# Performance work log

Hardware: AMD Instinct MI355X
Metric: run time of the kernel (lower is better)

The kernel has to match this reference:

```python
import jax, jax.numpy as jnp
import numpy as np

N_NODES = 50000
N_EDGES = 600000
D = 128
REL_DIM = 100
N_REL = 40
NEG_SLOPE = 0.2


def setup_inputs() -> dict:
    key = jax.random.key(0)
    ks = jax.random.split(key, 9)
    return {
        "node_features": jax.random.normal(ks[0], (N_NODES, D), jnp.float32),
        "edge_index": jax.random.randint(ks[1], (2, N_EDGES), 0, N_NODES, jnp.int64 if jax.config.jax_enable_x64 else jnp.int32),
        "edge_type": jax.random.randint(ks[2], (N_EDGES,), 0, N_REL, jnp.int32),
        "W": jax.random.normal(ks[3], (D, D), jnp.float32) * (1.0 / np.sqrt(D)),
        "W_r": jax.random.normal(ks[4], (REL_DIM, D), jnp.float32) * (1.0 / np.sqrt(REL_DIM)),
        "a": jax.random.normal(ks[5], (3 * D,), jnp.float32) * (1.0 / np.sqrt(3 * D)),
        "W_res": jax.random.normal(ks[6], (D, D), jnp.float32) * (1.0 / np.sqrt(D)),
        "b_res": jax.random.normal(ks[7], (D,), jnp.float32) * 0.01,
        "rel_emb": jax.random.normal(ks[8], (N_REL, REL_DIM), jnp.float32),
    }


def _segment_softmax(logits, seg_ids, num_segments):
    # numerically stable softmax over edges grouped by destination node
    seg_max = jax.ops.segment_max(logits, seg_ids, num_segments=num_segments)
    seg_max = jnp.where(jnp.isfinite(seg_max), seg_max, 0.0)
    e = jnp.exp(logits - seg_max[seg_ids])
    seg_sum = jax.ops.segment_sum(e, seg_ids, num_segments=num_segments)
    return e / (seg_sum[seg_ids] + 1e-16)


def reference(node_features, edge_index, edge_type, W, W_r, a, W_res, b_res, rel_emb):
    src = edge_index[0]  # x_j (source / message sender)
    dst = edge_index[1]  # x_i (target / aggregation index)

    h = node_features @ W                      # [N, D]
    h_rel = rel_emb[edge_type] @ W_r           # [E, D]
    h_src = h[src]                             # [E, D]
    h_dst = h[dst]                             # [E, D]

    # attention logit per edge: a . cat(W x_i, W x_j, W_r r_e), LeakyReLU(0.2)
    logit = h_dst @ a[:D] + h_src @ a[D:2 * D] + h_rel @ a[2 * D:]  # [E]
    logit = jax.nn.leaky_relu(logit, NEG_SLOPE)

    alpha = _segment_softmax(logit, dst, N_NODES)  # [E]

    agg = jax.ops.segment_sum(h_src * alpha[:, None], dst, num_segments=N_NODES)  # [N, D]

    out = agg + node_features @ W_res + b_res  # residual connection
    # LayerG: SELU then dropout (identity in eval mode)
    return jax.nn.selu(out)
```

## Files before the change

kernel.cpp:

```cpp
#include <hip/hip_runtime.h>
#include <hip/hip_bf16.h>

typedef __attribute__((ext_vector_type(8))) short bf16x8;
typedef __attribute__((ext_vector_type(4))) float f32x4;

#define LDS_STRIDE 528
#define CAP 64

__device__ __forceinline__ float waveSum(float v) {
    for (int d = 32; d; d >>= 1) v += __shfl_xor(v, d, 64);
    return v;
}
__device__ __forceinline__ unsigned short f2bf(float f) {
    union { float f; unsigned int u; } v; v.f = f;
    unsigned int r = (v.u + 0x7FFF + ((v.u >> 16) & 1)) >> 16;
    return (unsigned short)r;
}
__device__ __forceinline__ float bf2f(unsigned int hbits) {
    union { unsigned int u; float f; } v; v.u = hbits << 16;
    return v.f;
}

__global__ __launch_bounds__(256) void setup_kernel(
    int* __restrict__ counts, int N,
    const float* __restrict__ W, const float* __restrict__ W_res,
    unsigned short* __restrict__ WbPack,
    const float* __restrict__ W_r, const float* __restrict__ a,
    const float* __restrict__ rel_emb, float* __restrict__ rl,
    int n_rel, int rel_dim, int zb)
{
    __shared__ float a3[128];
    __shared__ float wa[128];
    int bid = blockIdx.x;
    int tid = threadIdx.x;
    if (bid < zb) {
        int i = bid * 256 + tid;
        if (i < N) counts[i] = 0;
        return;
    }
    if (bid < zb + 16) {
        int g = (bid - zb) * 256 + tid;
        int t = g >> 8;
        int s = (g >> 6) & 3;
        int lane = g & 63;
        int ncol = ((t & 7) << 4) + (lane & 15);
        int k0 = s * 32 + ((lane >> 4) << 3);
        const float* srcw = (t < 8) ? W : W_res;
        unsigned short* dst = WbPack + ((size_t)(t * 4 + s) * 64 + lane) * 8;
        #pragma unroll
        for (int j = 0; j < 8; ++j) dst[j] = f2bf(srcw[(size_t)(k0 + j) * 128 + ncol]);
        return;
    }
    if (tid < 128) {
        a3[tid] = a[256 + tid];
    }
    __syncthreads();
    if (tid < rel_dim) {
        float s = 0.f;
        for (int d = 0; d < 128; ++d) s += W_r[tid * 128 + d] * a3[d];
        wa[tid] = s;
    }
    __syncthreads();
    if (tid < n_rel) {
        float s = 0.f;
        for (int k = 0; k < rel_dim; ++k) s += rel_emb[tid * rel_dim + k] * wa[k];
        rl[tid] = s;
    }
}

__global__ __launch_bounds__(256) void gemm_dual_kernel(
    const float* __restrict__ X, const unsigned short* __restrict__ WbPack,
    const float* __restrict__ b_res, const float* __restrict__ a,
    unsigned short* __restrict__ hb, unsigned short* __restrict__ resb,
    float* __restrict__ p, float* __restrict__ q, int M)
{
    __shared__ __align__(16) unsigned char smem[64 * LDS_STRIDE];
    __shared__ float pq_s[128];
    const int tid = threadIdx.x;
    const int lane = tid & 63;
    const int wave = tid >> 6;
    const int rowbase = blockIdx.x * 64;
    const int c16 = lane & 15;
    const int kq = lane >> 4;

    if (tid < 128) pq_s[tid] = 0.f;

    bf16x8 wfrag[4][4];
    #pragma unroll
    for (int tt = 0; tt < 4; ++tt)
        #pragma unroll
        for (int s = 0; s < 4; ++s)
            wfrag[tt][s] = *(const bf16x8*)(WbPack + ((size_t)((wave * 4 + tt) * 4 + s) * 64 + lane) * 8);

    float bres[4];
    #pragma unroll
    for (int tt = 0; tt < 4; ++tt) {
        int t = wave * 4 + tt;
        bres[tt] = (t >= 8) ? b_res[(t - 8) * 16 + c16] : 0.f;
    }
    float pa[4], qa[4];
    #pragma unroll
    for (int tt = 0; tt < 4; ++tt) {
        int col = (wave * 4 + tt) * 16 + c16;
        pa[tt] = (wave < 2) ? a[col] : 0.f;
        qa[tt] = (wave < 2) ? a[128 + col] : 0.f;
    }

    #pragma unroll
    for (int j = 0; j < 8; ++j) {
        int ch = j * 256 + tid;
        int r = ch >> 5;
        int c = ch & 31;
        int gr = rowbase + r; if (gr >= M) gr = M - 1;
        float4 v = *(const float4*)(X + (size_t)gr * 128 + c * 4);
        unsigned int u0 = ((unsigned)f2bf(v.y) << 16) | f2bf(v.x);
        unsigned int u1 = ((unsigned)f2bf(v.w) << 16) | f2bf(v.z);
        *(uint2*)(smem + r * LDS_STRIDE + c * 8) = make_uint2(u0, u1);
    }
    __syncthreads();

    f32x4 acc[4][4];
    #pragma unroll
    for (int rt = 0; rt < 4; ++rt)
        #pragma unroll
        for (int tt = 0; tt < 4; ++tt) acc[rt][tt] = (f32x4){0.f, 0.f, 0.f, 0.f};

    #pragma unroll
    for (int s = 0; s < 4; ++s) {
        #pragma unroll
        for (int rt = 0; rt < 4; ++rt) {
            int row = rt * 16 + c16;
            bf16x8 af = *(const bf16x8*)(smem + row * LDS_STRIDE + s * 64 + kq * 16);
            #pragma unroll
            for (int tt = 0; tt < 4; ++tt)
                acc[rt][tt] = __builtin_amdgcn_mfma_f32_16x16x32_bf16(af, wfrag[tt][s], acc[rt][tt], 0, 0, 0);
        }
    }
    __syncthreads();

    if (wave < 2) {
        #pragma unroll
        for (int rt = 0; rt < 4; ++rt) {
            #pragma unroll
            for (int i = 0; i < 4; ++i) {
                float pp = 0.f, qq = 0.f;
                #pragma unroll
                for (int tt = 0; tt < 4; ++tt) {
                    pp += acc[rt][tt][i] * pa[tt];
                    qq += acc[rt][tt][i] * qa[tt];
                }
                #pragma unroll
                for (int d = 1; d < 16; d <<= 1) {
                    pp += __shfl_xor(pp, d, 64);
                    qq += __shfl_xor(qq, d, 64);
                }
                if (c16 == 0) {
                    int r = rt * 16 + kq * 4 + i;
                    atomicAdd(&pq_s[r], pp);
                    atomicAdd(&pq_s[64 + r], qq);
                }
            }
        }
    }

    #pragma unroll
    for (int rt = 0; rt < 4; ++rt) {
        #pragma unroll
        for (int tt = 0; tt < 4; ++tt) {
            int colall = (wave * 4 + tt) * 16 + c16;
            #pragma unroll
            for (int i = 0; i < 4; ++i) {
                int row = rt * 16 + kq * 4 + i;
                *(unsigned short*)(smem + row * LDS_STRIDE + colall * 2) = f2bf(acc[rt][tt][i] + bres[tt]);
            }
        }
    }
    __syncthreads();

    #pragma unroll
    for (int j = 0; j < 4; ++j) {
        int ch = j * 256 + tid;
        int r = ch >> 4;
        int c = ch & 15;
        int gr = rowbase + r;
        uint4 hv = *(const uint4*)(smem + r * LDS_STRIDE + c * 16);
        uint4 rv = *(const uint4*)(smem + r * LDS_STRIDE + 256 + c * 16);
        if (gr < M) {
            *(uint4*)(hb + (size_t)gr * 128 + c * 8) = hv;
            *(uint4*)(resb + (size_t)gr * 128 + c * 8) = rv;
        }
    }
    if (tid < 64) {
        int gr = rowbase + tid;
        if (gr < M) { p[gr] = pq_s[tid]; q[gr] = pq_s[64 + tid]; }
    }
}

__global__ __launch_bounds__(256) void edge_kernel(
    const int* __restrict__ src, const int* __restrict__ dst, const int* __restrict__ etype,
    int* __restrict__ counts, unsigned int* __restrict__ slots, int E)
{
    const int xcd = blockIdx.x & 7;
    const int stripe = blockIdx.x >> 3;
    const int base = stripe * 2048 + threadIdx.x;
    #pragma unroll
    for (int k = 0; k < 8; ++k) {
        int e = base + k * 256;
        if (e < E) {
            int d = dst[e];
            if (((d >> 2) & 7) == xcd) {
                int s = src[e];
                int t = etype[e];
                int rk = atomicAdd(&counts[d], 1);
                if (rk < CAP)
                    slots[(size_t)d * CAP + rk] = (unsigned int)s | ((unsigned int)t << 16);
            }
        }
    }
}

__global__ __launch_bounds__(256) void agg_kernel(
    const unsigned short* __restrict__ hb, const unsigned short* __restrict__ resb,
    const float* __restrict__ p, const float* __restrict__ q, const float* __restrict__ rl,
    const int* __restrict__ counts, const unsigned int* __restrict__ slots,
    float* __restrict__ out, int N, int n_rel)
{
    __shared__ float rls[64];
    if (threadIdx.x < n_rel) rls[threadIdx.x] = rl[threadIdx.x];
    __syncthreads();

    int node = blockIdx.x * 4 + (threadIdx.x >> 6);
    int lane = threadIdx.x & 63;
    if (node >= N) return;
    int nn = min(counts[node], CAP);

    float se = 0.f;
    int sv = 0;
    if (lane < nn) {
        unsigned int pk = slots[(size_t)node * CAP + lane];
        sv = (int)(pk & 0xffffu);
        int t = (int)(pk >> 16);
        float l = p[node] + q[sv] + rls[t];
        l = (l > 0.f) ? l : 0.2f * l;
        se = __expf(l);
    }
    float ssum = waveSum(se);
    float inv = 1.0f / (ssum + 1e-16f);

    float a0 = 0.f, a1 = 0.f;
    const unsigned short* hlane = hb + lane * 2;
    int j = 0;
    for (; j + 7 < nn; j += 8) {
        float w[8]; int r[8]; unsigned int v[8];
        #pragma unroll
        for (int u = 0; u < 8; ++u) { w[u] = __shfl(se, j + u); r[u] = __shfl(sv, j + u); }
        #pragma unroll
        for (int u = 0; u < 8; ++u) v[u] = *(const unsigned int*)(hlane + (size_t)r[u] * 128);
        #pragma unroll
        for (int u = 0; u < 8; ++u) {
            a0 += w[u] * bf2f(v[u] & 0xffff);
            a1 += w[u] * bf2f(v[u] >> 16);
        }
    }
    for (; j + 3 < nn; j += 4) {
        float w[4]; int r[4]; unsigned int v[4];
        #pragma unroll
        for (int u = 0; u < 4; ++u) { w[u] = __shfl(se, j + u); r[u] = __shfl(sv, j + u); }
        #pragma unroll
        for (int u = 0; u < 4; ++u) v[u] = *(const unsigned int*)(hlane + (size_t)r[u] * 128);
        #pragma unroll
        for (int u = 0; u < 4; ++u) {
            a0 += w[u] * bf2f(v[u] & 0xffff);
            a1 += w[u] * bf2f(v[u] >> 16);
        }
    }
    for (; j < nn; ++j) {
        float w = __shfl(se, j);
        int r = __shfl(sv, j);
        unsigned int v = *(const unsigned int*)(hlane + (size_t)r * 128);
        a0 += w * bf2f(v & 0xffff);
        a1 += w * bf2f(v >> 16);
    }

    a0 *= inv; a1 *= inv;

    unsigned int rv = __builtin_nontemporal_load((const unsigned int*)(resb + (size_t)node * 128 + lane * 2));
    float o0 = a0 + bf2f(rv & 0xffff), o1 = a1 + bf2f(rv >> 16);
    const float SC = 1.0507009873554805f, AL = 1.6732632423543772f;
    o0 = (o0 > 0.f) ? SC * o0 : SC * AL * (__expf(o0) - 1.f);
    o1 = (o1 > 0.f) ? SC * o1 : SC * AL * (__expf(o1) - 1.f);
    union { float f[2]; unsigned long long u; } ov;
    ov.f[0] = o0; ov.f[1] = o1;
    __builtin_nontemporal_store(ov.u, (unsigned long long*)(out + (size_t)node * 128 + lane * 2));
}

extern "C" void kernel_launch(void* const* d_in, const int* in_sizes, int n_in,
                              void* d_out, int out_size, void* d_ws, size_t ws_size,
                              hipStream_t stream)
{
    const float* X      = (const float*)d_in[0];
    const int*   ei     = (const int*)d_in[1];
    const int*   etype  = (const int*)d_in[2];
    const float* W      = (const float*)d_in[3];
    const float* W_r    = (const float*)d_in[4];
    const float* a      = (const float*)d_in[5];
    const float* W_res  = (const float*)d_in[6];
    const float* b_res  = (const float*)d_in[7];
    const float* rel_emb= (const float*)d_in[8];

    const int N = in_sizes[0] / 128;
    const int E = in_sizes[2];
    const int n_rel = in_sizes[8] / 100;
    const int* src = ei;
    const int* dst = ei + E;

    char* w = (char*)d_ws;
    auto alloc = [&](size_t bytes) -> void* {
        void* ptr = (void*)w;
        w += (bytes + 255) & ~(size_t)255;
        return ptr;
    };
    unsigned short* WbPack = (unsigned short*)alloc((size_t)16 * 4 * 64 * 8 * 2);
    unsigned short* hb     = (unsigned short*)alloc((size_t)N * 128 * 2);
    unsigned short* resb   = (unsigned short*)alloc((size_t)N * 128 * 2);
    float* p       = (float*)alloc((size_t)N * 4);
    float* q       = (float*)alloc((size_t)N * 4);
    float* rl      = (float*)alloc(64 * 4);
    int*   counts  = (int*)alloc((size_t)N * 4);
    unsigned int* slots = (unsigned int*)alloc((size_t)N * CAP * 4);
    float* out     = (float*)d_out;

    const int zb = (N + 255) / 256;
    const int gemm_blocks = (N + 63) / 64;
    const int node_wave_blocks = (N + 3) / 4;
    const int stripes = (E + 2047) / 2048;
    const int edge_blocks = stripes * 8;

    setup_kernel<<<zb + 17, 256, 0, stream>>>(counts, N, W, W_res, WbPack,
                                              W_r, a, rel_emb, rl, n_rel, 100, zb);
    gemm_dual_kernel<<<gemm_blocks, 256, 0, stream>>>(X, WbPack, b_res, a, hb, resb, p, q, N);
    edge_kernel<<<edge_blocks, 256, 0, stream>>>(src, dst, etype, counts, slots, E);
    agg_kernel<<<node_wave_blocks, 256, 0, stream>>>(hb, resb, p, q, rl, counts, slots, out, N, n_rel);
}
```

Measured before the change: 180.9 us.

## Process two nodes per wavefront in aggregation with 32-lane half-waves

The aggregation kernel now assigns each 32-lane half of a wavefront to its own destination node. Each lane gathers 4 bf16 features (8 bytes) per neighbor instead of 2, and the softmax weights are computed in chunks of 32 edges, with the sum reduced across the half-wave. With about 12 edges per node on average, most of the 64 lanes were idle during the weight computation, and the 4-byte gathers were narrow; this change targets both. The cost is a chunk loop for nodes with more than 32 edges, and the residual load is no longer marked nontemporal.

After: 175.2 us. -3.2%, faster.

```diff
diff --git a/kernel.cpp b/kernel.cpp
--- a/kernel.cpp
+++ b/kernel.cpp
@@ -7,10 +7,6 @@
 #define LDS_STRIDE 528
 #define CAP 64
 
-__device__ __forceinline__ float waveSum(float v) {
-    for (int d = 32; d; d >>= 1) v += __shfl_xor(v, d, 64);
-    return v;
-}
 __device__ __forceinline__ unsigned short f2bf(float f) {
     union { float f; unsigned int u; } v; v.f = f;
     unsigned int r = (v.u + 0x7FFF + ((v.u >> 16) & 1)) >> 16;
@@ -229,69 +225,88 @@
     if (threadIdx.x < n_rel) rls[threadIdx.x] = rl[threadIdx.x];
     __syncthreads();
 
-    int node = blockIdx.x * 4 + (threadIdx.x >> 6);
-    int lane = threadIdx.x & 63;
+    const int tid = threadIdx.x;
+    const int lane = tid & 63;
+    const int sub = lane & 31;
+    const int shbase = lane & 32;
+    int node = blockIdx.x * 8 + ((tid >> 6) << 1) + (lane >> 5);
     if (node >= N) return;
     int nn = min(counts[node], CAP);
 
-    float se = 0.f;
-    int sv = 0;
-    if (lane < nn) {
-        unsigned int pk = slots[(size_t)node * CAP + lane];
-        sv = (int)(pk & 0xffffu);
-        int t = (int)(pk >> 16);
-        float l = p[node] + q[sv] + rls[t];
-        l = (l > 0.f) ? l : 0.2f * l;
-        se = __expf(l);
-    }
-    float ssum = waveSum(se);
+    float pnode = p[node];
+    float a0 = 0.f, a1 = 0.f, a2 = 0.f, a3 = 0.f;
+    float ssum = 0.f;
+    const unsigned short* hsub = hb + sub * 4;
+
+    for (int c = 0; c < nn; c += 32) {
+        int m = min(32, nn - c);
+        float se = 0.f;
+        int sv = 0;
+        if (sub < m) {
+            unsigned int pk = slots[(size_t)node * CAP + c + sub];
+            sv = (int)(pk & 0xffffu);
+            int t = (int)(pk >> 16);
+            float l = pnode + q[sv] + rls[t];
+            l = (l > 0.f) ? l : 0.2f * l;
+            se = __expf(l);
+        }
+        ssum += se;
+
+        int j = 0;
+        for (; j + 7 < m; j += 8) {
+            float w[8]; int r[8]; uint2 v[8];
+            #pragma unroll
+            for (int u = 0; u < 8; ++u) { w[u] = __shfl(se, shbase + j + u); r[u] = __shfl(sv, shbase + j + u); }
+            #pragma unroll
+            for (int u = 0; u < 8; ++u) v[u] = *(const uint2*)(hsub + (size_t)r[u] * 128);
+            #pragma unroll
+            for (int u = 0; u < 8; ++u) {
+                a0 += w[u] * bf2f(v[u].x & 0xffff);
+                a1 += w[u] * bf2f(v[u].x >> 16);
+                a2 += w[u] * bf2f(v[u].y & 0xffff);
+                a3 += w[u] * bf2f(v[u].y >> 16);
+            }
+        }
+        for (; j + 3 < m; j += 4) {
+            float w[4]; int r[4]; uint2 v[4];
+            #pragma unroll
+            for (int u = 0; u < 4; ++u) { w[u] = __shfl(se, shbase + j + u); r[u] = __shfl(sv, shbase + j + u); }
+            #pragma unroll
+            for (int u = 0; u < 4; ++u) v[u] = *(const uint2*)(hsub + (size_t)r[u] * 128);
+            #pragma unroll
+            for (int u = 0; u < 4; ++u) {
+                a0 += w[u] * bf2f(v[u].x & 0xffff);
+                a1 += w[u] * bf2f(v[u].x >> 16);
+                a2 += w[u] * bf2f(v[u].y & 0xffff);
+                a3 += w[u] * bf2f(v[u].y >> 16);
+            }
+        }
+        for (; j < m; ++j) {
+            float w = __shfl(se, shbase + j);
+            int r = __shfl(sv, shbase + j);
+            uint2 v = *(const uint2*)(hsub + (size_t)r * 128);
+            a0 += w * bf2f(v.x & 0xffff);
+            a1 += w * bf2f(v.x >> 16);
+            a2 += w * bf2f(v.y & 0xffff);
+            a3 += w * bf2f(v.y >> 16);
+        }
+    }
+
+    #pragma unroll
+    for (int d = 1; d < 32; d <<= 1) ssum += __shfl_xor(ssum, d, 64);
     float inv = 1.0f / (ssum + 1e-16f);
-
-    float a0 = 0.f, a1 = 0.f;
-    const unsigned short* hlane = hb + lane * 2;
-    int j = 0;
-    for (; j + 7 < nn; j += 8) {
-        float w[8]; int r[8]; unsigned int v[8];
-        #pragma unroll
-        for (int u = 0; u < 8; ++u) { w[u] = __shfl(se, j + u); r[u] = __shfl(sv, j + u); }
-        #pragma unroll
-        for (int u = 0; u < 8; ++u) v[u] = *(const unsigned int*)(hlane + (size_t)r[u] * 128);
-        #pragma unroll
-        for (int u = 0; u < 8; ++u) {
-            a0 += w[u] * bf2f(v[u] & 0xffff);
-            a1 += w[u] * bf2f(v[u] >> 16);
-        }
-    }
-    for (; j + 3 < nn; j += 4) {
-        float w[4]; int r[4]; unsigned int v[4];
-        #pragma unroll
-        for (int u = 0; u < 4; ++u) { w[u] = __shfl(se, j + u); r[u] = __shfl(sv, j + u); }
-        #pragma unroll
-        for (int u = 0; u < 4; ++u) v[u] = *(const unsigned int*)(hlane + (size_t)r[u] * 128);
-        #pragma unroll
-        for (int u = 0; u < 4; ++u) {
-            a0 += w[u] * bf2f(v[u] & 0xffff);
-            a1 += w[u] * bf2f(v[u] >> 16);
-        }
-    }
-    for (; j < nn; ++j) {
-        float w = __shfl(se, j);
-        int r = __shfl(sv, j);
-        unsigned int v = *(const unsigned int*)(hlane + (size_t)r * 128);
-        a0 += w * bf2f(v & 0xffff);
-        a1 += w * bf2f(v >> 16);
-    }
-
-    a0 *= inv; a1 *= inv;
-
-    unsigned int rv = __builtin_nontemporal_load((const unsigned int*)(resb + (size_t)node * 128 + lane * 2));
-    float o0 = a0 + bf2f(rv & 0xffff), o1 = a1 + bf2f(rv >> 16);
+    a0 *= inv; a1 *= inv; a2 *= inv; a3 *= inv;
+
+    uint2 rv = *(const uint2*)(resb + (size_t)node * 128 + sub * 4);
+    float o0 = a0 + bf2f(rv.x & 0xffff), o1 = a1 + bf2f(rv.x >> 16);
+    float o2 = a2 + bf2f(rv.y & 0xffff), o3 = a3 + bf2f(rv.y >> 16);
     const float SC = 1.0507009873554805f, AL = 1.6732632423543772f;
     o0 = (o0 > 0.f) ? SC * o0 : SC * AL * (__expf(o0) - 1.f);
     o1 = (o1 > 0.f) ? SC * o1 : SC * AL * (__expf(o1) - 1.f);
-    union { float f[2]; unsigned long long u; } ov;
-    ov.f[0] = o0; ov.f[1] = o1;
-    __builtin_nontemporal_store(ov.u, (unsigned long long*)(out + (size_t)node * 128 + lane * 2));
+    o2 = (o2 > 0.f) ? SC * o2 : SC * AL * (__expf(o2) - 1.f);
+    o3 = (o3 > 0.f) ? SC * o3 : SC * AL * (__expf(o3) - 1.f);
+    f32x4 ov = (f32x4){o0, o1, o2, o3};
+    __builtin_nontemporal_store(ov, (f32x4*)(out + (size_t)node * 128 + sub * 4));
 }
 
 extern "C" void kernel_launch(void* const* d_in, const int* in_sizes, int n_in,
@@ -332,7 +347,7 @@
 
     const int zb = (N + 255) / 256;
     const int gemm_blocks = (N + 63) / 64;
-    const int node_wave_blocks = (N + 3) / 4;
+    const int agg_blocks = (N + 7) / 8;
     const int stripes = (E + 2047) / 2048;
     const int edge_blocks = stripes * 8;
 
@@ -340,5 +355,5 @@
                                               W_r, a, rel_emb, rl, n_rel, 100, zb);
     gemm_dual_kernel<<<gemm_blocks, 256, 0, stream>>>(X, WbPack, b_res, a, hb, resb, p, q, N);
     edge_kernel<<<edge_blocks, 256, 0, stream>>>(src, dst, etype, counts, slots, E);
-    agg_kernel<<<node_wave_blocks, 256, 0, stream>>>(hb, resb, p, q, rl, counts, slots, out, N, n_rel);
-}
+    agg_kernel<<<agg_blocks, 256, 0, stream>>>(hb, resb, p, q, rl, counts, slots, out, N, n_rel);
+}
```
